# Kernel tuning notes

Measured on AMD Instinct MI355X. Metric: run time of the kernel, lower is better.

The kernel has to match this reference:

```python
import jax, jax.numpy as jnp
import numpy as np

N_Q = 16
N_K = 16
D_QK = 64
D_V = 64
# torch module default scale=1.0 saturates softmax at feature width 1024;
# we use the conventional sqrt(d) scale for well-conditioned numerics.
SCALE = 32.0  # sqrt(N_Q * D_QK)
DROPOUT_P = 0.0  # dropout is identity at p=0


def setup_inputs() -> dict:
    key = jax.random.key(0)
    kq, kk, kv = jax.random.split(key, 3)
    S = 8192
    return {
        "query": jax.random.normal(kq, (S, N_Q, D_QK), dtype=jnp.float32),
        "key": jax.random.normal(kk, (S, N_K, D_QK), dtype=jnp.float32),
        "value": jax.random.normal(kv, (S, N_K, D_V), dtype=jnp.float32),
    }


def reference(query, key, value):
    # Flatten trailing (head, dim) into one feature axis, as the torch view does.
    q = query.reshape(-1, N_Q * D_QK)            # [S_q, 1024]
    k = key.reshape(-1, N_K * D_QK)              # [S_k, 1024]
    v = value.reshape(-1, N_K * D_V)             # [S_k, 1024]
    scores = jnp.matmul(q, k.T) / SCALE          # [S_q, S_k]
    attn = jax.nn.softmax(scores, axis=-1)       # dropout_p=0 -> identity
    out = jnp.matmul(attn, v)                    # [S_q, 1024]
    return out.reshape(query.shape[:-1] + (-1,))  # [S_q, N_Q, D_V]
```

## Files before the change

kernel.cpp:

```cpp
#include <hip/hip_runtime.h>
#include <hip/hip_bf16.h>


typedef __bf16 bf16x8 __attribute__((ext_vector_type(8)));
typedef float f32x4 __attribute__((ext_vector_type(4)));
typedef const __attribute__((address_space(1))) unsigned int* as1p;
typedef __attribute__((address_space(3))) unsigned int* as3p;
typedef unsigned short u16;

__device__ __forceinline__ u16 f2bf(float x) {
  unsigned u = __float_as_uint(x);
  u += 0x7fffu + ((u >> 16) & 1u);
  return (u16)(u >> 16);
}
__device__ __forceinline__ float bf2f(u16 b) { return __uint_as_float(((unsigned)b) << 16); }
__device__ __forceinline__ unsigned pack2(float lo, float hi) {
  return (unsigned)f2bf(lo) | ((unsigned)f2bf(hi) << 16);
}

#define BAR()   do { __builtin_amdgcn_s_barrier(); asm volatile("" ::: "memory"); } while (0)
#define LGKM0() do { asm volatile("s_waitcnt lgkmcnt(0)" ::: "memory"); __builtin_amdgcn_sched_barrier(0); } while (0)
#define VM(n)   do { asm volatile("s_waitcnt vmcnt(" #n ")" ::: "memory"); __builtin_amdgcn_sched_barrier(0); } while (0)

__global__ __launch_bounds__(256) void cvt_bf16(const float* __restrict__ in,
                                                unsigned short* __restrict__ out) {
  const size_t i = (size_t)blockIdx.x * 256 + threadIdx.x;
  const float4* p = (const float4*)in + i * 2;
  float4 a = p[0], b = p[1];
  uint4 o;
  o.x = pack2(a.x, a.y);
  o.y = pack2(a.z, a.w);
  o.z = pack2(b.x, b.y);
  o.w = pack2(b.z, b.w);
  ((uint4*)out)[i] = o;
}

__global__ __launch_bounds__(256) void transpose_bf16(const float* __restrict__ V,
                                                      unsigned short* __restrict__ VT) {
  __shared__ float t[64][65];
  const int rb = blockIdx.x * 64;
  const int cb = blockIdx.y * 64;
  const int tid = threadIdx.x;
#pragma unroll
  for (int it = 0; it < 4; ++it) {
    int r = it * 16 + (tid >> 4);
    int c = (tid & 15) * 4;
    float4 x = *(const float4*)(V + (size_t)(rb + r) * 1024 + cb + c);
    t[r][c] = x.x; t[r][c + 1] = x.y; t[r][c + 2] = x.z; t[r][c + 3] = x.w;
  }
  __syncthreads();
  const int j = tid & 63;
  const int c0 = (tid >> 6) * 16;
#pragma unroll
  for (int i = 0; i < 16; ++i) {
    int c = c0 + i;
    VT[(size_t)(cb + c) * 8192 + rb + j] = f2bf(t[j][c]);
  }
}

template <int BM, int OUTMODE, int DEC>
__global__ __launch_bounds__(512, 2) void gemm_fr(const u16* __restrict__ A,
                                                  const u16* __restrict__ B,
                                                  void* __restrict__ Cv,
                                                  const float* __restrict__ inv,
                                                  float* __restrict__ partials,
                                                  int K, int ldc, float scale) {
  constexpr int MF = BM / 32;
  constexpr int MH = MF / 2;
  constexpr int LA = BM / 64;
  constexpr int LB = 4;
  constexpr int LPT = LA + LB;
  constexpr int ABUF = BM * 128;
  constexpr int BBUF = 32768;
  constexpr int BUFSZ = ABUF + BBUF;
  __shared__ __align__(1024) char smem[2 * BUFSZ];

  const int tid = threadIdx.x;
  const int lane = tid & 63, wave = tid >> 6;
  const int wr = wave >> 2, wc = wave & 3;
  const int lan15 = lane & 15, g = lane >> 4, l7 = lane & 7;

  const int nwg = gridDim.x;
  const int wg = (blockIdx.x & 7) * (nwg >> 3) + (blockIdx.x >> 3);

  int bm0, bn0;
  if constexpr (DEC == 0) {
    const int r = wg & 255;
    bm0 = (r >> 3) * 256;
    bn0 = (((wg >> 8) << 3) | (r & 7)) * 256;
  } else {
    bm0 = (wg & 63) * BM;
    bn0 = (wg >> 6) * 256;
  }

  const int sr = tid >> 3;
  const int scb = ((tid & 7) ^ (sr & 7)) * 8;
  const u16* Ags = A + (size_t)(bm0 + sr) * K + scb;
  const u16* Bgs = B + (size_t)(bn0 + sr) * K + scb;

  const int sa0 = ((0 + g) ^ l7) * 16;
  const int sa1 = ((4 + g) ^ l7) * 16;
  const int abase = (wr * (BM / 2) + lan15) * 128;
  const int bbase = ABUF + (wc * 64 + lan15) * 128;

  f32x4 acc[MF][4];
#pragma unroll
  for (int m = 0; m < MF; ++m)
#pragma unroll
    for (int n = 0; n < 4; ++n) acc[m][n] = f32x4{0.f, 0.f, 0.f, 0.f};

  const int nt = K >> 6;

  auto ISSUE = [&](int t) {
    const int bb = (t & 1) * BUFSZ;
    const size_t ko = (size_t)t * 64;
#pragma unroll
    for (int j = 0; j < LA; ++j)
      __builtin_amdgcn_global_load_lds((as1p)(Ags + (size_t)j * 64 * K + ko),
                                       (as3p)(smem + bb + j * 8192 + tid * 16), 16, 0, 0);
#pragma unroll
    for (int j = 0; j < LB; ++j)
      __builtin_amdgcn_global_load_lds((as1p)(Bgs + (size_t)j * 64 * K + ko),
                                       (as3p)(smem + bb + ABUF + j * 8192 + tid * 16), 16, 0, 0);
  };

  ISSUE(0);
  ISSUE(1);
  if constexpr (LPT == 8) { VM(8); } else { VM(6); }
  BAR();

  for (int t = 0; t < nt; ++t) {
    const char* bp = smem + (t & 1) * BUFSZ;

    bf16x8 a0[MH][2], b0[4][2], a1[MH][2];
#pragma unroll
    for (int m = 0; m < MH; ++m) {
      a0[m][0] = *(const bf16x8*)(bp + abase + m * 2048 + sa0);
      a0[m][1] = *(const bf16x8*)(bp + abase + m * 2048 + sa1);
    }
#pragma unroll
    for (int n = 0; n < 4; ++n) {
      b0[n][0] = *(const bf16x8*)(bp + bbase + n * 2048 + sa0);
      b0[n][1] = *(const bf16x8*)(bp + bbase + n * 2048 + sa1);
    }
#pragma unroll
    for (int m = 0; m < MH; ++m) {
      a1[m][0] = *(const bf16x8*)(bp + abase + (MH + m) * 2048 + sa0);
      a1[m][1] = *(const bf16x8*)(bp + abase + (MH + m) * 2048 + sa1);
    }

    __builtin_amdgcn_s_setprio(1);
#pragma unroll
    for (int m = 0; m < MH; ++m)
#pragma unroll
      for (int n = 0; n < 2; ++n)
#pragma unroll
        for (int ks = 0; ks < 2; ++ks)
          acc[m][n] = __builtin_amdgcn_mfma_f32_16x16x32_bf16(a0[m][ks], b0[n][ks], acc[m][n], 0, 0, 0);
#pragma unroll
    for (int m = 0; m < MH; ++m)
#pragma unroll
      for (int n = 0; n < 2; ++n)
#pragma unroll
        for (int ks = 0; ks < 2; ++ks)
          acc[m][2 + n] = __builtin_amdgcn_mfma_f32_16x16x32_bf16(a0[m][ks], b0[2 + n][ks], acc[m][2 + n], 0, 0, 0);
#pragma unroll
    for (int m = 0; m < MH; ++m)
#pragma unroll
      for (int n = 0; n < 2; ++n)
#pragma unroll
        for (int ks = 0; ks < 2; ++ks)
          acc[MH + m][n] = __builtin_amdgcn_mfma_f32_16x16x32_bf16(a1[m][ks], b0[n][ks], acc[MH + m][n], 0, 0, 0);
#pragma unroll
    for (int m = 0; m < MH; ++m)
#pragma unroll
      for (int n = 0; n < 2; ++n)
#pragma unroll
        for (int ks = 0; ks < 2; ++ks)
          acc[MH + m][2 + n] = __builtin_amdgcn_mfma_f32_16x16x32_bf16(a1[m][ks], b0[2 + n][ks], acc[MH + m][2 + n], 0, 0, 0);
    __builtin_amdgcn_s_setprio(0);

    LGKM0();
    BAR();

    const bool st = (t + 2 < nt);
    if (st) ISSUE(t + 2);
    if (t + 1 < nt) {
      if (st) {
        if constexpr (LPT == 8) { VM(8); } else { VM(6); }
      } else {
        VM(0);
      }
    }
    BAR();
  }

  const int c0 = bn0 + wc * 64 + lan15;
  if constexpr (OUTMODE == 0) {
    u16* C = (u16*)Cv;
    const int cb4 = (bn0 >> 8) * 4 + wc;
#pragma unroll
    for (int m = 0; m < MF; ++m)
#pragma unroll
      for (int r = 0; r < 4; ++r) {
        const int row = bm0 + wr * (BM / 2) + m * 16 + g * 4 + r;
        float part = 0.f;
#pragma unroll
        for (int n = 0; n < 4; ++n) {
          float v = __expf(acc[m][n][r] * scale);
          C[(size_t)row * ldc + c0 + n * 16] = f2bf(v);
          part += v;
        }
        part += __shfl_xor(part, 1, 64);
        part += __shfl_xor(part, 2, 64);
        part += __shfl_xor(part, 4, 64);
        part += __shfl_xor(part, 8, 64);
        if (lan15 == 0) partials[(size_t)row * 128 + cb4] = part;
      }
  } else {
    float* C = (float*)Cv;
#pragma unroll
    for (int m = 0; m < MF; ++m)
#pragma unroll
      for (int r = 0; r < 4; ++r) {
        const int row = bm0 + wr * (BM / 2) + m * 16 + g * 4 + r;
        const float iv = inv ? inv[row] : 1.0f;
#pragma unroll
        for (int n = 0; n < 4; ++n)
          C[(size_t)row * ldc + c0 + n * 16] = acc[m][n][r] * iv;
      }
  }
}

__global__ __launch_bounds__(256) void rowinv(const float* __restrict__ partials,
                                              float* __restrict__ inv) {
  const int row = blockIdx.x * 256 + threadIdx.x;
  const float4* p = (const float4*)(partials + (size_t)row * 128);
  float s = 0.f;
#pragma unroll
  for (int j = 0; j < 32; ++j) {
    float4 v = p[j];
    s += (v.x + v.y) + (v.z + v.w);
  }
  inv[row] = 1.0f / s;
}

__global__ __launch_bounds__(256) void normalize_inplace(u16* __restrict__ E) {
  __shared__ float red[4];
  u16* row = E + (size_t)blockIdx.x * 8192;
  const int tid = threadIdx.x;
  float f[32];
  float s = 0.f;
#pragma unroll
  for (int c = 0; c < 4; ++c) {
    uint4 v = *((const uint4*)row + c * 256 + tid);
    unsigned u[4] = {v.x, v.y, v.z, v.w};
#pragma unroll
    for (int q = 0; q < 4; ++q) {
      f[c * 8 + q * 2] = bf2f((u16)(u[q] & 0xffffu));
      f[c * 8 + q * 2 + 1] = bf2f((u16)(u[q] >> 16));
      s += f[c * 8 + q * 2] + f[c * 8 + q * 2 + 1];
    }
  }
#pragma unroll
  for (int off = 32; off; off >>= 1) s += __shfl_xor(s, off, 64);
  if ((tid & 63) == 0) red[tid >> 6] = s;
  __syncthreads();
  const float iv = 1.0f / ((red[0] + red[1]) + (red[2] + red[3]));
#pragma unroll
  for (int c = 0; c < 4; ++c) {
    uint4 o;
    o.x = pack2(f[c * 8 + 0] * iv, f[c * 8 + 1] * iv);
    o.y = pack2(f[c * 8 + 2] * iv, f[c * 8 + 3] * iv);
    o.z = pack2(f[c * 8 + 4] * iv, f[c * 8 + 5] * iv);
    o.w = pack2(f[c * 8 + 6] * iv, f[c * 8 + 7] * iv);
    *((uint4*)row + c * 256 + tid) = o;
  }
}

extern "C" void kernel_launch(void* const* d_in, const int* in_sizes, int n_in,
                              void* d_out, int out_size, void* d_ws, size_t ws_size,
                              hipStream_t stream) {
  const float* Q = (const float*)d_in[0];
  const float* K = (const float*)d_in[1];
  const float* V = (const float*)d_in[2];

  char* ws = (char*)d_ws;
  u16* S = (u16*)ws;
  u16* VT = (u16*)(ws + (size_t)134217728);
  float* partials = (float*)(ws + (size_t)134217728 + 16777216);
  float* inv = (float*)(ws + (size_t)134217728 + 16777216 + 4194304);
  const bool haveInv =
      ws_size >= (size_t)134217728 + 16777216 + 4194304 + 32768;

  u16* Qb = (u16*)d_out;
  u16* Kb = Qb + 8388608;

  cvt_bf16<<<4096, 256, 0, stream>>>(Q, Qb);
  cvt_bf16<<<4096, 256, 0, stream>>>(K, Kb);
  transpose_bf16<<<dim3(128, 16), 256, 0, stream>>>(V, VT);

  gemm_fr<256, 0, 0><<<1024, 512, 0, stream>>>(
      Qb, Kb, S, nullptr, haveInv ? partials : (float*)(ws + 134217728 + 16777216),
      1024, 8192, 1.0f / 32.0f);

  if (haveInv) {
    rowinv<<<32, 256, 0, stream>>>(partials, inv);
    gemm_fr<128, 1, 1><<<256, 512, 0, stream>>>(
        S, VT, d_out, inv, nullptr, 8192, 1024, 1.0f);
  } else {
    normalize_inplace<<<8192, 256, 0, stream>>>(S);
    gemm_fr<128, 1, 1><<<256, 512, 0, stream>>>(
        S, VT, d_out, nullptr, nullptr, 8192, 1024, 1.0f);
  }
}
```

Before: 320.7 us.

## Restructure GEMM mainloop into 4-stage K=32 pipeline with split A/B loads

The GEMM main loop drops from K-step 64 with double buffering to K-step 32 with a four-buffer ring, prefetching three tiles ahead. A and B tile loads are issued separately, each interleaved with one half of the MFMA work, and barriers sit between the LDS reads and the MFMAs. The intent is to hide global-to-LDS latency and spread memory traffic across the iteration. The cost is twice as many loop iterations and barriers and more complex vmcnt bookkeeping, with a changed swizzle and row mapping that could introduce correctness or bank-conflict problems.

```diff
diff --git a/kernel.cpp b/kernel.cpp
--- a/kernel.cpp
+++ b/kernel.cpp
@@ -19,7 +19,6 @@
 }
 
 #define BAR()   do { __builtin_amdgcn_s_barrier(); asm volatile("" ::: "memory"); } while (0)
-#define LGKM0() do { asm volatile("s_waitcnt lgkmcnt(0)" ::: "memory"); __builtin_amdgcn_sched_barrier(0); } while (0)
 #define VM(n)   do { asm volatile("s_waitcnt vmcnt(" #n ")" ::: "memory"); __builtin_amdgcn_sched_barrier(0); } while (0)
 
 __global__ __launch_bounds__(256) void cvt_bf16(const float* __restrict__ in,
@@ -59,7 +58,7 @@
 }
 
 template <int BM, int OUTMODE, int DEC>
-__global__ __launch_bounds__(512, 2) void gemm_fr(const u16* __restrict__ A,
+__global__ __launch_bounds__(512, 2) void gemm_dp(const u16* __restrict__ A,
                                                   const u16* __restrict__ B,
                                                   void* __restrict__ Cv,
                                                   const float* __restrict__ inv,
@@ -67,13 +66,11 @@
                                                   int K, int ldc, float scale) {
   constexpr int MF = BM / 32;
   constexpr int MH = MF / 2;
-  constexpr int LA = BM / 64;
-  constexpr int LB = 4;
-  constexpr int LPT = LA + LB;
-  constexpr int ABUF = BM * 128;
-  constexpr int BBUF = 32768;
-  constexpr int BUFSZ = ABUF + BBUF;
-  __shared__ __align__(1024) char smem[2 * BUFSZ];
+  constexpr int LA = BM / 128;
+  constexpr int LPT = LA + 2;
+  constexpr int ABUFB = BM * 64;
+  constexpr int BUFSZ = ABUFB + 16384;
+  __shared__ __align__(1024) char smem[4 * BUFSZ];
 
   const int tid = threadIdx.x;
   const int lane = tid & 63, wave = tid >> 6;
@@ -82,7 +79,6 @@
 
   const int nwg = gridDim.x;
   const int wg = (blockIdx.x & 7) * (nwg >> 3) + (blockIdx.x >> 3);
-
   int bm0, bn0;
   if constexpr (DEC == 0) {
     const int r = wg & 255;
@@ -93,15 +89,28 @@
     bn0 = (wg >> 6) * 256;
   }
 
-  const int sr = tid >> 3;
-  const int scb = ((tid & 7) ^ (sr & 7)) * 8;
-  const u16* Ags = A + (size_t)(bm0 + sr) * K + scb;
-  const u16* Bgs = B + (size_t)(bn0 + sr) * K + scb;
-
-  const int sa0 = ((0 + g) ^ l7) * 16;
-  const int sa1 = ((4 + g) ^ l7) * 16;
-  const int abase = (wr * (BM / 2) + lan15) * 128;
-  const int bbase = ABUF + (wc * 64 + lan15) * 128;
+  const int rho = tid >> 3;
+  const int s8 = tid & 7;
+  const int xx = s8 ^ (rho & 7);
+  const int cc = xx & 3, hh = xx >> 2;
+
+  const u16* AgJ[LA];
+#pragma unroll
+  for (int j = 0; j < LA; ++j) {
+    const int rA = j * 64 + rho + (BM / 2) * hh;
+    AgJ[j] = A + (size_t)(bm0 + rA) * K + cc * 8;
+  }
+  const u16* BgJ[2];
+#pragma unroll
+  for (int j = 0; j < 2; ++j) {
+    const int rB = j * 64 + rho + 128 * hh;
+    BgJ[j] = B + (size_t)(bn0 + rB) * K + cc * 8;
+  }
+
+  const int saA = ((g + 4 * wr) ^ l7) * 16;
+  const int saB = ((g + 4 * (wc >> 1)) ^ l7) * 16;
+  const int brow = ABUFB + ((wc & 1) * 64 + lan15) * 128 + saB;
+  const int arow = lan15 * 128 + saA;
 
   f32x4 acc[MF][4];
 #pragma unroll
@@ -109,88 +118,66 @@
 #pragma unroll
     for (int n = 0; n < 4; ++n) acc[m][n] = f32x4{0.f, 0.f, 0.f, 0.f};
 
-  const int nt = K >> 6;
-
-  auto ISSUE = [&](int t) {
-    const int bb = (t & 1) * BUFSZ;
-    const size_t ko = (size_t)t * 64;
+  const int nt = K >> 5;
+
+  auto ISSUE_A = [&](int t) {
+    char* bb = smem + (t & 3) * BUFSZ;
 #pragma unroll
     for (int j = 0; j < LA; ++j)
-      __builtin_amdgcn_global_load_lds((as1p)(Ags + (size_t)j * 64 * K + ko),
-                                       (as3p)(smem + bb + j * 8192 + tid * 16), 16, 0, 0);
-#pragma unroll
-    for (int j = 0; j < LB; ++j)
-      __builtin_amdgcn_global_load_lds((as1p)(Bgs + (size_t)j * 64 * K + ko),
-                                       (as3p)(smem + bb + ABUF + j * 8192 + tid * 16), 16, 0, 0);
+      __builtin_amdgcn_global_load_lds((as1p)(AgJ[j] + t * 32),
+                                       (as3p)(bb + j * 8192 + tid * 16), 16, 0, 0);
   };
-
-  ISSUE(0);
-  ISSUE(1);
-  if constexpr (LPT == 8) { VM(8); } else { VM(6); }
+  auto ISSUE_B = [&](int t) {
+    char* bb = smem + (t & 3) * BUFSZ + ABUFB;
+#pragma unroll
+    for (int j = 0; j < 2; ++j)
+      __builtin_amdgcn_global_load_lds((as1p)(BgJ[j] + t * 32),
+                                       (as3p)(bb + j * 8192 + tid * 16), 16, 0, 0);
+  };
+
+  ISSUE_A(0); ISSUE_B(0);
+  ISSUE_A(1); ISSUE_B(1);
+  ISSUE_A(2); ISSUE_B(2);
+  if constexpr (LPT == 4) { VM(8); } else { VM(6); }
   BAR();
 
+  bf16x8 a[MH], b[4];
   for (int t = 0; t < nt; ++t) {
-    const char* bp = smem + (t & 1) * BUFSZ;
-
-    bf16x8 a0[MH][2], b0[4][2], a1[MH][2];
-#pragma unroll
-    for (int m = 0; m < MH; ++m) {
-      a0[m][0] = *(const bf16x8*)(bp + abase + m * 2048 + sa0);
-      a0[m][1] = *(const bf16x8*)(bp + abase + m * 2048 + sa1);
-    }
-#pragma unroll
-    for (int n = 0; n < 4; ++n) {
-      b0[n][0] = *(const bf16x8*)(bp + bbase + n * 2048 + sa0);
-      b0[n][1] = *(const bf16x8*)(bp + bbase + n * 2048 + sa1);
-    }
-#pragma unroll
-    for (int m = 0; m < MH; ++m) {
-      a1[m][0] = *(const bf16x8*)(bp + abase + (MH + m) * 2048 + sa0);
-      a1[m][1] = *(const bf16x8*)(bp + abase + (MH + m) * 2048 + sa1);
-    }
-
+    const char* bp = smem + (t & 3) * BUFSZ;
+    const bool st = (t + 3 < nt);
+
+    if (st) ISSUE_A(t + 3);
+#pragma unroll
+    for (int m = 0; m < MH; ++m) a[m] = *(const bf16x8*)(bp + arow + m * 2048);
+#pragma unroll
+    for (int n = 0; n < 4; ++n) b[n] = *(const bf16x8*)(bp + brow + n * 2048);
+    BAR();
     __builtin_amdgcn_s_setprio(1);
 #pragma unroll
     for (int m = 0; m < MH; ++m)
 #pragma unroll
-      for (int n = 0; n < 2; ++n)
-#pragma unroll
-        for (int ks = 0; ks < 2; ++ks)
-          acc[m][n] = __builtin_amdgcn_mfma_f32_16x16x32_bf16(a0[m][ks], b0[n][ks], acc[m][n], 0, 0, 0);
+      for (int n = 0; n < 4; ++n)
+        acc[m][n] = __builtin_amdgcn_mfma_f32_16x16x32_bf16(a[m], b[n], acc[m][n], 0, 0, 0);
+    __builtin_amdgcn_s_setprio(0);
+    BAR();
+
+    if (st) ISSUE_B(t + 3);
+#pragma unroll
+    for (int m = 0; m < MH; ++m) a[m] = *(const bf16x8*)(bp + arow + (MH + m) * 2048);
+    BAR();
+    __builtin_amdgcn_s_setprio(1);
 #pragma unroll
     for (int m = 0; m < MH; ++m)
 #pragma unroll
-      for (int n = 0; n < 2; ++n)
-#pragma unroll
-        for (int ks = 0; ks < 2; ++ks)
-          acc[m][2 + n] = __builtin_amdgcn_mfma_f32_16x16x32_bf16(a0[m][ks], b0[2 + n][ks], acc[m][2 + n], 0, 0, 0);
-#pragma unroll
-    for (int m = 0; m < MH; ++m)
-#pragma unroll
-      for (int n = 0; n < 2; ++n)
-#pragma unroll
-        for (int ks = 0; ks < 2; ++ks)
-          acc[MH + m][n] = __builtin_amdgcn_mfma_f32_16x16x32_bf16(a1[m][ks], b0[n][ks], acc[MH + m][n], 0, 0, 0);
-#pragma unroll
-    for (int m = 0; m < MH; ++m)
-#pragma unroll
-      for (int n = 0; n < 2; ++n)
-#pragma unroll
-        for (int ks = 0; ks < 2; ++ks)
-          acc[MH + m][2 + n] = __builtin_amdgcn_mfma_f32_16x16x32_bf16(a1[m][ks], b0[2 + n][ks], acc[MH + m][2 + n], 0, 0, 0);
+      for (int n = 0; n < 4; ++n)
+        acc[MH + m][n] = __builtin_amdgcn_mfma_f32_16x16x32_bf16(a[m], b[n], acc[MH + m][n], 0, 0, 0);
     __builtin_amdgcn_s_setprio(0);
-
-    LGKM0();
-    BAR();
-
-    const bool st = (t + 2 < nt);
-    if (st) ISSUE(t + 2);
-    if (t + 1 < nt) {
-      if (st) {
-        if constexpr (LPT == 8) { VM(8); } else { VM(6); }
-      } else {
-        VM(0);
-      }
+    if (st) {
+      if constexpr (LPT == 4) { VM(8); } else { VM(6); }
+    } else if (t + 2 < nt) {
+      if constexpr (LPT == 4) { VM(4); } else { VM(3); }
+    } else if (t + 1 < nt) {
+      VM(0);
     }
     BAR();
   }
@@ -300,17 +287,17 @@
   cvt_bf16<<<4096, 256, 0, stream>>>(K, Kb);
   transpose_bf16<<<dim3(128, 16), 256, 0, stream>>>(V, VT);
 
-  gemm_fr<256, 0, 0><<<1024, 512, 0, stream>>>(
+  gemm_dp<256, 0, 0><<<1024, 512, 0, stream>>>(
       Qb, Kb, S, nullptr, haveInv ? partials : (float*)(ws + 134217728 + 16777216),
       1024, 8192, 1.0f / 32.0f);
 
   if (haveInv) {
     rowinv<<<32, 256, 0, stream>>>(partials, inv);
-    gemm_fr<128, 1, 1><<<256, 512, 0, stream>>>(
+    gemm_dp<128, 1, 1><<<256, 512, 0, stream>>>(
         S, VT, d_out, inv, nullptr, 8192, 1024, 1.0f);
   } else {
     normalize_inplace<<<8192, 256, 0, stream>>>(S);
-    gemm_fr<128, 1, 1><<<256, 512, 0, stream>>>(
+    gemm_dp<128, 1, 1><<<256, 512, 0, stream>>>(
         S, VT, d_out, nullptr, nullptr, 8192, 1024, 1.0f);
   }
 }
```

New measurement: 335.6 us. 4.7% more time.

## Load GEMM B operand as prepacked MFMA fragments directly into registers, bypassing LDS

Applied to the files above, without the earlier changes.

Replaces the K convert and V transpose kernels with kernels that write K and V in per-lane MFMA fragment order as bf16. The GEMM then loads B fragments from global memory straight into registers, double-buffered across K-steps. Only A is staged through LDS, which halves shared memory per block and removes one barrier per iteration. The cost is that B is no longer shared across waves through LDS, so global/L2 traffic for B goes up, and register pressure rises.

```diff
diff --git a/kernel.cpp b/kernel.cpp
--- a/kernel.cpp
+++ b/kernel.cpp
@@ -19,6 +19,7 @@
 }
 
 #define BAR()   do { __builtin_amdgcn_s_barrier(); asm volatile("" ::: "memory"); } while (0)
+#define SCHED0() __builtin_amdgcn_sched_barrier(0)
 #define LGKM0() do { asm volatile("s_waitcnt lgkmcnt(0)" ::: "memory"); __builtin_amdgcn_sched_barrier(0); } while (0)
 #define VM(n)   do { asm volatile("s_waitcnt vmcnt(" #n ")" ::: "memory"); __builtin_amdgcn_sched_barrier(0); } while (0)
 
@@ -35,45 +36,77 @@
   ((uint4*)out)[i] = o;
 }
 
-__global__ __launch_bounds__(256) void transpose_bf16(const float* __restrict__ V,
-                                                      unsigned short* __restrict__ VT) {
-  __shared__ float t[64][65];
-  const int rb = blockIdx.x * 64;
-  const int cb = blockIdx.y * 64;
+__global__ __launch_bounds__(256) void kfrag_write(const float* __restrict__ K,
+                                                   uint4* __restrict__ Kf) {
+  __shared__ float lds[16][257];
+  const int nb = blockIdx.x;
+  const int ktg = blockIdx.y;
   const int tid = threadIdx.x;
 #pragma unroll
-  for (int it = 0; it < 4; ++it) {
-    int r = it * 16 + (tid >> 4);
-    int c = (tid & 15) * 4;
-    float4 x = *(const float4*)(V + (size_t)(rb + r) * 1024 + cb + c);
-    t[r][c] = x.x; t[r][c + 1] = x.y; t[r][c + 2] = x.z; t[r][c + 3] = x.w;
+  for (int p = 0; p < 4; ++p) {
+    const int row = p * 4 + (tid >> 6);
+    const int c = (tid & 63) * 4;
+    float4 v = *(const float4*)(K + (size_t)(nb * 16 + row) * 1024 + ktg * 256 + c);
+    lds[row][c] = v.x; lds[row][c + 1] = v.y; lds[row][c + 2] = v.z; lds[row][c + 3] = v.w;
   }
   __syncthreads();
-  const int j = tid & 63;
-  const int c0 = (tid >> 6) * 16;
-#pragma unroll
-  for (int i = 0; i < 16; ++i) {
-    int c = c0 + i;
-    VT[(size_t)(cb + c) * 8192 + rb + j] = f2bf(t[j][c]);
-  }
-}
-
-template <int BM, int OUTMODE, int DEC>
-__global__ __launch_bounds__(512, 2) void gemm_fr(const u16* __restrict__ A,
-                                                  const u16* __restrict__ B,
+#pragma unroll
+  for (int w = 0; w < 2; ++w) {
+    const int o = w * 256 + tid;
+    const int kt_loc = o >> 7, ks = (o >> 6) & 1, lane = o & 63;
+    const int nl = lane & 15;
+    const int kb = kt_loc * 64 + ks * 32 + ((lane >> 4) & 3) * 8;
+    uint4 q;
+    q.x = pack2(lds[nl][kb + 0], lds[nl][kb + 1]);
+    q.y = pack2(lds[nl][kb + 2], lds[nl][kb + 3]);
+    q.z = pack2(lds[nl][kb + 4], lds[nl][kb + 5]);
+    q.w = pack2(lds[nl][kb + 6], lds[nl][kb + 7]);
+    Kf[(((size_t)nb * 16 + ktg * 4 + kt_loc) * 2 + ks) * 64 + lane] = q;
+  }
+}
+
+__global__ __launch_bounds__(256) void vfrag_write(const float* __restrict__ V,
+                                                   uint4* __restrict__ Vf) {
+  __shared__ float lds[256][17];
+  const int nb = blockIdx.x;
+  const int ktg = blockIdx.y;
+  const int tid = threadIdx.x;
+#pragma unroll
+  for (int p = 0; p < 4; ++p) {
+    const int row = p * 64 + (tid >> 2);
+    const int cf = (tid & 3) * 4;
+    float4 v = *(const float4*)(V + (size_t)(ktg * 256 + row) * 1024 + nb * 16 + cf);
+    lds[row][cf] = v.x; lds[row][cf + 1] = v.y; lds[row][cf + 2] = v.z; lds[row][cf + 3] = v.w;
+  }
+  __syncthreads();
+#pragma unroll
+  for (int w = 0; w < 2; ++w) {
+    const int o = w * 256 + tid;
+    const int kt_loc = o >> 7, ks = (o >> 6) & 1, lane = o & 63;
+    const int cl = lane & 15;
+    const int kvb = kt_loc * 64 + ks * 32 + ((lane >> 4) & 3) * 8;
+    uint4 q;
+    q.x = pack2(lds[kvb + 0][cl], lds[kvb + 1][cl]);
+    q.y = pack2(lds[kvb + 2][cl], lds[kvb + 3][cl]);
+    q.z = pack2(lds[kvb + 4][cl], lds[kvb + 5][cl]);
+    q.w = pack2(lds[kvb + 6][cl], lds[kvb + 7][cl]);
+    Vf[(((size_t)nb * 128 + ktg * 4 + kt_loc) * 2 + ks) * 64 + lane] = q;
+  }
+}
+
+template <int BM, int KTSPAN, int OUTMODE, int DEC>
+__global__ __launch_bounds__(512, 2) void gemm_bd(const u16* __restrict__ A,
+                                                  const uint4* __restrict__ Bf,
                                                   void* __restrict__ Cv,
                                                   const float* __restrict__ inv,
                                                   float* __restrict__ partials,
                                                   int K, int ldc, float scale) {
   constexpr int MF = BM / 32;
   constexpr int MH = MF / 2;
-  constexpr int LA = BM / 64;
-  constexpr int LB = 4;
-  constexpr int LPT = LA + LB;
+  constexpr int LA = BM / 128;
+  constexpr int LAJ = BM / 64;
   constexpr int ABUF = BM * 128;
-  constexpr int BBUF = 32768;
-  constexpr int BUFSZ = ABUF + BBUF;
-  __shared__ __align__(1024) char smem[2 * BUFSZ];
+  __shared__ __align__(1024) char smem[2 * ABUF];
 
   const int tid = threadIdx.x;
   const int lane = tid & 63, wave = tid >> 6;
@@ -82,7 +115,6 @@
 
   const int nwg = gridDim.x;
   const int wg = (blockIdx.x & 7) * (nwg >> 3) + (blockIdx.x >> 3);
-
   int bm0, bn0;
   if constexpr (DEC == 0) {
     const int r = wg & 255;
@@ -96,12 +128,12 @@
   const int sr = tid >> 3;
   const int scb = ((tid & 7) ^ (sr & 7)) * 8;
   const u16* Ags = A + (size_t)(bm0 + sr) * K + scb;
-  const u16* Bgs = B + (size_t)(bn0 + sr) * K + scb;
 
   const int sa0 = ((0 + g) ^ l7) * 16;
   const int sa1 = ((4 + g) ^ l7) * 16;
   const int abase = (wr * (BM / 2) + lan15) * 128;
-  const int bbase = ABUF + (wc * 64 + lan15) * 128;
+
+  const int nb0 = (bn0 >> 4) + wc * 4;
 
   f32x4 acc[MF][4];
 #pragma unroll
@@ -111,88 +143,76 @@
 
   const int nt = K >> 6;
 
-  auto ISSUE = [&](int t) {
-    const int bb = (t & 1) * BUFSZ;
+  auto ISSUE_A = [&](int t) {
+    char* bb = smem + (t & 1) * ABUF;
     const size_t ko = (size_t)t * 64;
 #pragma unroll
-    for (int j = 0; j < LA; ++j)
+    for (int j = 0; j < LAJ; ++j)
       __builtin_amdgcn_global_load_lds((as1p)(Ags + (size_t)j * 64 * K + ko),
-                                       (as3p)(smem + bb + j * 8192 + tid * 16), 16, 0, 0);
-#pragma unroll
-    for (int j = 0; j < LB; ++j)
-      __builtin_amdgcn_global_load_lds((as1p)(Bgs + (size_t)j * 64 * K + ko),
-                                       (as3p)(smem + bb + ABUF + j * 8192 + tid * 16), 16, 0, 0);
+                                       (as3p)(bb + j * 8192 + tid * 16), 16, 0, 0);
   };
 
-  ISSUE(0);
-  ISSUE(1);
-  if constexpr (LPT == 8) { VM(8); } else { VM(6); }
+  auto LOADB = [&](int t, bf16x8 (&bq)[4][2]) {
+    const int tc = (t < nt) ? t : (nt - 1);
+#pragma unroll
+    for (int n = 0; n < 4; ++n)
+#pragma unroll
+      for (int ks = 0; ks < 2; ++ks) {
+        const uint4 q = Bf[(((size_t)(nb0 + n) * KTSPAN + tc) * 2 + ks) * 64 + lane];
+        bq[n][ks] = *(const bf16x8*)&q;
+      }
+  };
+
+  bf16x8 bA[4][2], bB[4][2];
+
+  ISSUE_A(0);
+  SCHED0();
+  LOADB(0, bA);
+  VM(8);
   BAR();
 
-  for (int t = 0; t < nt; ++t) {
-    const char* bp = smem + (t & 1) * BUFSZ;
-
-    bf16x8 a0[MH][2], b0[4][2], a1[MH][2];
+  auto TILE = [&](int t, bf16x8 (&bc)[4][2], bf16x8 (&bn_)[4][2]) {
+    const char* bp = smem + (t & 1) * ABUF;
+    if (t + 1 < nt) ISSUE_A(t + 1);
+    SCHED0();
+    LOADB(t + 1, bn_);
+    bf16x8 a[MH][2];
 #pragma unroll
     for (int m = 0; m < MH; ++m) {
-      a0[m][0] = *(const bf16x8*)(bp + abase + m * 2048 + sa0);
-      a0[m][1] = *(const bf16x8*)(bp + abase + m * 2048 + sa1);
+      a[m][0] = *(const bf16x8*)(bp + abase + m * 2048 + sa0);
+      a[m][1] = *(const bf16x8*)(bp + abase + m * 2048 + sa1);
     }
-#pragma unroll
-    for (int n = 0; n < 4; ++n) {
-      b0[n][0] = *(const bf16x8*)(bp + bbase + n * 2048 + sa0);
-      b0[n][1] = *(const bf16x8*)(bp + bbase + n * 2048 + sa1);
+    __builtin_amdgcn_s_setprio(1);
+#pragma unroll
+    for (int m = 0; m < MH; ++m)
+#pragma unroll
+      for (int n = 0; n < 4; ++n)
+#pragma unroll
+        for (int ks = 0; ks < 2; ++ks)
+          acc[m][n] = __builtin_amdgcn_mfma_f32_16x16x32_bf16(a[m][ks], bc[n][ks], acc[m][n], 0, 0, 0);
+    __builtin_amdgcn_s_setprio(0);
+#pragma unroll
+    for (int m = 0; m < MH; ++m) {
+      a[m][0] = *(const bf16x8*)(bp + abase + (MH + m) * 2048 + sa0);
+      a[m][1] = *(const bf16x8*)(bp + abase + (MH + m) * 2048 + sa1);
     }
-#pragma unroll
-    for (int m = 0; m < MH; ++m) {
-      a1[m][0] = *(const bf16x8*)(bp + abase + (MH + m) * 2048 + sa0);
-      a1[m][1] = *(const bf16x8*)(bp + abase + (MH + m) * 2048 + sa1);
-    }
-
     __builtin_amdgcn_s_setprio(1);
 #pragma unroll
     for (int m = 0; m < MH; ++m)
 #pragma unroll
-      for (int n = 0; n < 2; ++n)
+      for (int n = 0; n < 4; ++n)
 #pragma unroll
         for (int ks = 0; ks < 2; ++ks)
-          acc[m][n] = __builtin_amdgcn_mfma_f32_16x16x32_bf16(a0[m][ks], b0[n][ks], acc[m][n], 0, 0, 0);
-#pragma unroll
-    for (int m = 0; m < MH; ++m)
-#pragma unroll
-      for (int n = 0; n < 2; ++n)
-#pragma unroll
-        for (int ks = 0; ks < 2; ++ks)
-          acc[m][2 + n] = __builtin_amdgcn_mfma_f32_16x16x32_bf16(a0[m][ks], b0[2 + n][ks], acc[m][2 + n], 0, 0, 0);
-#pragma unroll
-    for (int m = 0; m < MH; ++m)
-#pragma unroll
-      for (int n = 0; n < 2; ++n)
-#pragma unroll
-        for (int ks = 0; ks < 2; ++ks)
-          acc[MH + m][n] = __builtin_amdgcn_mfma_f32_16x16x32_bf16(a1[m][ks], b0[n][ks], acc[MH + m][n], 0, 0, 0);
-#pragma unroll
-    for (int m = 0; m < MH; ++m)
-#pragma unroll
-      for (int n = 0; n < 2; ++n)
-#pragma unroll
-        for (int ks = 0; ks < 2; ++ks)
-          acc[MH + m][2 + n] = __builtin_amdgcn_mfma_f32_16x16x32_bf16(a1[m][ks], b0[2 + n][ks], acc[MH + m][2 + n], 0, 0, 0);
+          acc[MH + m][n] = __builtin_amdgcn_mfma_f32_16x16x32_bf16(a[m][ks], bc[n][ks], acc[MH + m][n], 0, 0, 0);
     __builtin_amdgcn_s_setprio(0);
-
     LGKM0();
+    if (t + 1 < nt) { VM(8); } else { VM(0); }
     BAR();
-
-    const bool st = (t + 2 < nt);
-    if (st) ISSUE(t + 2);
-    if (t + 1 < nt) {
-      if (st) {
-        if constexpr (LPT == 8) { VM(8); } else { VM(6); }
-      } else {
-        VM(0);
-      }
-    }
-    BAR();
+  };
+
+  for (int t = 0; t < nt; t += 2) {
+    TILE(t, bA, bB);
+    TILE(t + 1, bB, bA);
   }
 
   const int c0 = bn0 + wc * 64 + lan15;
@@ -287,30 +307,30 @@
 
   char* ws = (char*)d_ws;
   u16* S = (u16*)ws;
-  u16* VT = (u16*)(ws + (size_t)134217728);
+  uint4* Vf = (uint4*)(ws + (size_t)134217728);
   float* partials = (float*)(ws + (size_t)134217728 + 16777216);
   float* inv = (float*)(ws + (size_t)134217728 + 16777216 + 4194304);
   const bool haveInv =
       ws_size >= (size_t)134217728 + 16777216 + 4194304 + 32768;
 
   u16* Qb = (u16*)d_out;
-  u16* Kb = Qb + 8388608;
+  uint4* Kf = (uint4*)((char*)d_out + 16777216);
 
   cvt_bf16<<<4096, 256, 0, stream>>>(Q, Qb);
-  cvt_bf16<<<4096, 256, 0, stream>>>(K, Kb);
-  transpose_bf16<<<dim3(128, 16), 256, 0, stream>>>(V, VT);
-
-  gemm_fr<256, 0, 0><<<1024, 512, 0, stream>>>(
-      Qb, Kb, S, nullptr, haveInv ? partials : (float*)(ws + 134217728 + 16777216),
+  kfrag_write<<<dim3(512, 4), 256, 0, stream>>>(K, Kf);
+  vfrag_write<<<dim3(64, 32), 256, 0, stream>>>(V, Vf);
+
+  gemm_bd<256, 16, 0, 0><<<1024, 512, 0, stream>>>(
+      Qb, Kf, S, nullptr, haveInv ? partials : (float*)(ws + 134217728 + 16777216),
       1024, 8192, 1.0f / 32.0f);
 
   if (haveInv) {
     rowinv<<<32, 256, 0, stream>>>(partials, inv);
-    gemm_fr<128, 1, 1><<<256, 512, 0, stream>>>(
-        S, VT, d_out, inv, nullptr, 8192, 1024, 1.0f);
+    gemm_bd<128, 128, 1, 1><<<256, 512, 0, stream>>>(
+        S, Vf, d_out, inv, nullptr, 8192, 1024, 1.0f);
   } else {
     normalize_inplace<<<8192, 256, 0, stream>>>(S);
-    gemm_fr<128, 1, 1><<<256, 512, 0, stream>>>(
-        S, VT, d_out, nullptr, nullptr, 8192, 1024, 1.0f);
-  }
-}
+    gemm_bd<128, 128, 1, 1><<<256, 512, 0, stream>>>(
+        S, Vf, d_out, nullptr, nullptr, 8192, 1024, 1.0f);
+  }
+}
```

New measurement: 334.9 us. +4.4%, slower.
